# Kernel optimization log

Measured on AMD Instinct MI355X. Metric: run time of the kernel, lower is better.

Reference implementation:

```python
import jax, jax.numpy as jnp
import numpy as np

N = 100_000   # nodes
E = 3_200_000 # edges
F = 13        # input features
H = 64        # hidden dim
G = 512       # graphs in batch
C = 2         # output classes
BN_EPS = 1e-5


def _linear(key, fan_in, fan_out):
    kw, kb = jax.random.split(key)
    bound = 1.0 / np.sqrt(fan_in)
    W = jax.random.uniform(kw, (fan_in, fan_out), jnp.float32, -bound, bound)
    b = jax.random.uniform(kb, (fan_out,), jnp.float32, -bound, bound)
    return W, b


def _conv_params(key, fin, fout):
    k1, k2, k3 = jax.random.split(key, 3)
    W1, b1 = _linear(k1, fin, fout)
    W2, b2 = _linear(k2, fout, fout)
    gamma = jnp.ones((fout,), jnp.float32)
    beta = jnp.zeros((fout,), jnp.float32)
    mean = jax.random.normal(k3, (fout,), jnp.float32) * 0.1
    var = jnp.ones((fout,), jnp.float32)
    return W1, b1, gamma, beta, mean, var, W2, b2


def setup_inputs() -> dict:
    key = jax.random.key(0)
    ks = jax.random.split(key, 10)
    x = jax.random.normal(ks[0], (N, F), jnp.float32)
    src = jax.random.randint(ks[1], (E,), 0, N, jnp.int32)
    dst = jax.random.randint(ks[2], (E,), 0, N, jnp.int32)
    batch = jnp.sort(jax.random.randint(ks[3], (N,), 0, G, jnp.int32))
    inp = {"x": x, "src": src, "dst": dst, "batch": batch}
    for i, name in enumerate(["c1", "c2", "c3"]):
        fin = F if i == 0 else H
        W1, b1, g, be, m, v, W2, b2 = _conv_params(ks[4 + i], fin, H)
        inp.update({f"{name}_W1": W1, f"{name}_b1": b1, f"{name}_g": g,
                    f"{name}_be": be, f"{name}_m": m, f"{name}_v": v,
                    f"{name}_W2": W2, f"{name}_b2": b2})
    inp["fc1_W"], inp["fc1_b"] = _linear(ks[7], 3 * H, 3 * H)
    inp["fc2_W"], inp["fc2_b"] = _linear(ks[8], 3 * H, C)
    return inp


def _mlp(h, W1, b1, g, be, m, v, W2, b2):
    # Linear -> BatchNorm1d (inference, running stats) -> ReLU -> Linear -> ReLU
    h = h @ W1 + b1
    h = (h - m) * jax.lax.rsqrt(v + BN_EPS) * g + be
    h = jax.nn.relu(h)
    return jax.nn.relu(h @ W2 + b2)


def _gin_conv(x, src, dst, mlp_params):
    # GINConv with eps=0: MLP(x + sum_{j->i} x_j) via scatter-add over edges
    agg = jax.ops.segment_sum(x[src], dst, num_segments=N)
    return _mlp(x + agg, *mlp_params)


def reference(x, src, dst, batch,
              c1_W1, c1_b1, c1_g, c1_be, c1_m, c1_v, c1_W2, c1_b2,
              c2_W1, c2_b1, c2_g, c2_be, c2_m, c2_v, c2_W2, c2_b2,
              c3_W1, c3_b1, c3_g, c3_be, c3_m, c3_v, c3_W2, c3_b2,
              fc1_W, fc1_b, fc2_W, fc2_b):
    h1 = jax.nn.relu(_gin_conv(x, src, dst, (c1_W1, c1_b1, c1_g, c1_be, c1_m, c1_v, c1_W2, c1_b2)))
    h2 = jax.nn.relu(_gin_conv(h1, src, dst, (c2_W1, c2_b1, c2_g, c2_be, c2_m, c2_v, c2_W2, c2_b2)))
    h3 = jax.nn.relu(_gin_conv(h2, src, dst, (c3_W1, c3_b1, c3_g, c3_be, c3_m, c3_v, c3_W2, c3_b2)))
    p1 = jax.ops.segment_sum(h1, batch, num_segments=G)
    p2 = jax.ops.segment_sum(h2, batch, num_segments=G)
    p3 = jax.ops.segment_sum(h3, batch, num_segments=G)
    h = jnp.concatenate([p1, p2, p3], axis=1)  # [G, 3H]
    h = jax.nn.relu(h @ fc1_W + fc1_b)
    # Dropout is identity in eval mode
    h = h @ fc2_W + fc2_b
    return jax.nn.log_softmax(h, axis=-1)
```

## Files before the change

kernel.cpp:

```cpp
#include <hip/hip_runtime.h>

#define NNODES 100000
#define NEDGES 3200000
#define NF 13
#define NFP 16
#define NG 512
#define BN_EPS 1e-5f
#define NTILES (NNODES / 16)
#define CAP 72

#define BSH 9
#define NBUCK ((NNODES + 511) / 512)
#define RCAP 18500
#define PTILE 4096
#define NPBLK ((NEDGES + PTILE - 1) / PTILE)

#define NCHUNK ((NNODES + 63) / 64)
#define NPTASK (3 * NCHUNK)

typedef __attribute__((ext_vector_type(8))) _Float16 f16x8;
typedef __attribute__((ext_vector_type(4))) _Float16 f16x4;
typedef __attribute__((ext_vector_type(4))) float f32x4;

__device__ __forceinline__ unsigned short f2h(float f) {
    union { _Float16 h; unsigned short u; } c;
    c.h = (_Float16)f;
    return c.u;
}
__device__ __forceinline__ float h2f(unsigned short u) {
    union { _Float16 h; unsigned short u; } c;
    c.u = u;
    return (float)c.h;
}

__device__ __forceinline__ f16x8 shfl_xor8(f16x8 v, int m) {
    union { f16x8 h; int i[4]; } a, b;
    a.h = v;
#pragma unroll
    for (int k = 0; k < 4; ++k) b.i[k] = __shfl_xor(a.i[k], m, 64);
    return b.h;
}
__device__ __forceinline__ f16x4 shfl_xor4(f16x4 v, int m) {
    union { f16x4 h; int i[2]; } a, b;
    a.h = v;
#pragma unroll
    for (int k = 0; k < 2; ++k) b.i[k] = __shfl_xor(a.i[k], m, 64);
    return b.h;
}

__launch_bounds__(256)
__global__ void partition_kernel(const int* __restrict__ src, const int* __restrict__ dst,
                                 int* __restrict__ gcount, int* __restrict__ pairbuf) {
    __shared__ int lhist[NBUCK];
    __shared__ int lbase[NBUCK];
    __shared__ int lpos[NBUCK];
    int t = threadIdx.x;
    int base = blockIdx.x * PTILE;
    int cnt = NEDGES - base; if (cnt > PTILE) cnt = PTILE;

    int v[PTILE / 256], b[PTILE / 256];
#pragma unroll
    for (int j = 0; j < PTILE / 256; ++j) {
        int i = t + j * 256;
        if (i < cnt) {
            int d = __builtin_nontemporal_load(dst + base + i);
            int s = __builtin_nontemporal_load(src + base + i);
            b[j] = d >> BSH;
            v[j] = ((d & 511) << 17) | s;
        } else b[j] = -1;
    }
    if (t < NBUCK) lhist[t] = 0;
    __syncthreads();
#pragma unroll
    for (int j = 0; j < PTILE / 256; ++j)
        if (b[j] >= 0) atomicAdd(&lhist[b[j]], 1);
    __syncthreads();
    if (t < NBUCK) {
        lbase[t] = atomicAdd(&gcount[t], lhist[t]);
        lpos[t] = 0;
    }
    __syncthreads();
#pragma unroll
    for (int j = 0; j < PTILE / 256; ++j) {
        if (b[j] >= 0) {
            int p = atomicAdd(&lpos[b[j]], 1);
            pairbuf[(size_t)b[j] * RCAP + lbase[b[j]] + p] = v[j];
        }
    }
}

__launch_bounds__(512)
__global__ void bucket_scatter_kernel(const int* __restrict__ pairbuf,
                                      const int* __restrict__ gcount,
                                      int* __restrict__ cursor, int* __restrict__ csr) {
    __shared__ int lcnt[512];
    int bk = blockIdx.x;
    int lo = bk << BSH;
    int cnt = gcount[bk];
    if (threadIdx.x < 512) lcnt[threadIdx.x] = 0;
    __syncthreads();
    const int* pb = pairbuf + (size_t)bk * RCAP;
    for (int i = threadIdx.x; i < cnt; i += 512) {
        int p = pb[i];
        int s = p & 0x1FFFF;
        int dl = p >> 17;
        int pos = atomicAdd(&lcnt[dl], 1);
        csr[(size_t)(lo + dl) * CAP + pos] = s;
    }
    __syncthreads();
    int n = lo + threadIdx.x;
    if (threadIdx.x < 512 && n < NNODES) cursor[n] = n * CAP + lcnt[threadIdx.x];
}

__global__ void cvt_x_kernel(const float* __restrict__ x, unsigned short* __restrict__ xh) {
    const int total = NNODES * NFP;
    int idx = blockIdx.x * blockDim.x + threadIdx.x;
    int stride = gridDim.x * blockDim.x;
    for (int i = idx; i < total; i += stride) {
        int n = i >> 4;
        int f = i & 15;
        xh[i] = (f < NF) ? f2h(x[n * NF + f]) : (unsigned short)0;
    }
}

__global__ void build_frags_kernel(const float* __restrict__ w10, const float* __restrict__ w20,
                                   const float* __restrict__ w11, const float* __restrict__ w21,
                                   const float* __restrict__ w12, const float* __restrict__ w22,
                                   unsigned short* __restrict__ wfrag) {
    int tid = blockIdx.x * blockDim.x + threadIdx.x;
    if (tid >= 3072) return;
    int layer = tid >> 10;
    int rem = tid & 1023;
    int mat = rem >> 9;
    int tile = (rem >> 7) & 3;
    int chunk = (rem >> 6) & 1;
    int lane = rem & 63;
    int quad = lane >> 4, n = lane & 15;
    const float* W = (layer == 0) ? (mat ? w20 : w10)
                   : (layer == 1) ? (mat ? w21 : w11)
                                  : (mat ? w22 : w12);
    int K = (layer == 0 && mat == 0) ? NF : 64;
    unsigned short* o = wfrag + ((size_t)tid) * 8;
#pragma unroll
    for (int j = 0; j < 8; ++j) {
        int k = chunk * 32 + quad * 8 + j;
        float val = (k < K) ? W[k * 64 + tile * 16 + n] : 0.f;
        o[j] = f2h(val);
    }
}

template <int FSTR, int RL, int UNROLL, int PADZ>
__launch_bounds__(256, 8)
__global__ void agg_vec_kernel(const unsigned short* __restrict__ xin,
                               const int* __restrict__ cursor,
                               const int* __restrict__ csr,
                               unsigned short* __restrict__ y) {
    const int EPG = 64 / RL;
    int lane = threadIdx.x & 63;
    int g = lane / RL;
    int r = lane % RL;
    int wave = (blockIdx.x * blockDim.x + threadIdx.x) >> 6;
    int nw = (gridDim.x * blockDim.x) >> 6;

    for (int n = wave; n < NNODES; n += nw) {
        int beg = n * CAP;
        int end = cursor[n];
        f16x4 acc = {0, 0, 0, 0};
        if (g == 0)
            acc = *(const f16x4*)&xin[n * FSTR + r * 4];
        int j = beg;
        const int STEP = UNROLL * EPG;
        for (; j + STEP <= end; j += STEP) {
#pragma unroll
            for (int t = 0; t < UNROLL; ++t) {
                int i0 = csr[j + t * EPG + g];
                acc += *(const f16x4*)&xin[i0 * FSTR + r * 4];
            }
        }
        for (; j < end; j += EPG) {
            int e = j + g;
            if (e < end) {
                int i0 = csr[e];
                acc += *(const f16x4*)&xin[i0 * FSTR + r * 4];
            }
        }
#pragma unroll
        for (int m = RL; m < 64; m <<= 1) acc += shfl_xor4(acc, m);
        if (g == 0) {
            *(f16x4*)&y[n * 64 + r * 4] = acc;
        } else if (PADZ && g == 1) {
            f16x4 z = {0, 0, 0, 0};
            *(f16x4*)&y[n * 64 + 16 + r * 4] = z;
        }
    }
}

__launch_bounds__(256, 8)
__global__ void agg_vec8_kernel(const unsigned short* __restrict__ xin,
                                const int* __restrict__ cursor,
                                const int* __restrict__ csr,
                                unsigned short* __restrict__ y) {
    int lane = threadIdx.x & 63;
    int g = lane >> 3;
    int r = lane & 7;
    int wave = (blockIdx.x * blockDim.x + threadIdx.x) >> 6;
    int nw = (gridDim.x * blockDim.x) >> 6;

    for (int n = wave; n < NNODES; n += nw) {
        int beg = n * CAP;
        int end = cursor[n];
        f16x8 acc = {0, 0, 0, 0, 0, 0, 0, 0};
        if (g == 0)
            acc = *(const f16x8*)&xin[(size_t)n * 64 + r * 8];
        int j = beg;
        for (; j + 16 <= end; j += 16) {
#pragma unroll
            for (int t = 0; t < 2; ++t) {
                int i0 = csr[j + t * 8 + g];
                acc += *(const f16x8*)&xin[(size_t)i0 * 64 + r * 8];
            }
        }
        for (; j < end; j += 8) {
            int e = j + g;
            if (e < end) {
                int i0 = csr[e];
                acc += *(const f16x8*)&xin[(size_t)i0 * 64 + r * 8];
            }
        }
#pragma unroll
        for (int m = 8; m < 64; m <<= 1) acc += shfl_xor8(acc, m);
        if (g == 0) *(f16x8*)&y[(size_t)n * 64 + r * 8] = acc;
    }
}

template <int KC1>
__launch_bounds__(256)
__global__ void mlp_mfma_kernel(const unsigned short* __restrict__ yh,
                                const unsigned short* __restrict__ wfrag,
                                const float* __restrict__ b1, const float* __restrict__ g,
                                const float* __restrict__ be, const float* __restrict__ m,
                                const float* __restrict__ v,  const float* __restrict__ b2,
                                unsigned short* __restrict__ hout) {
    __shared__ __align__(16) unsigned short zs[4][16 * 72];
    int lane = threadIdx.x & 63;
    int wid = threadIdx.x >> 6;
    int quad = lane >> 4;
    int n16 = lane & 15;

    const f16x8* wf = (const f16x8*)wfrag;
    f16x8 w1f[4][2], w2f[4][2];
#pragma unroll
    for (int t = 0; t < 4; ++t) {
#pragma unroll
        for (int c = 0; c < 2; ++c) {
            w1f[t][c] = wf[((0 * 4 + t) * 2 + c) * 64 + lane];
            w2f[t][c] = wf[((1 * 4 + t) * 2 + c) * 64 + lane];
        }
    }
    float scaleF[4], shiftF[4], b2F[4];
#pragma unroll
    for (int t = 0; t < 4; ++t) {
        int f = t * 16 + n16;
        float sc = g[f] * rsqrtf(v[f] + BN_EPS);
        scaleF[t] = sc;
        shiftF[t] = (b1[f] - m[f]) * sc + be[f];
        b2F[t] = b2[f];
    }

    unsigned short* zrow = &zs[wid][0];
    int ntiles = gridDim.x * 4;
    for (int tile = blockIdx.x * 4 + wid; tile < NTILES; tile += ntiles) {
        int nodebase = tile * 16;
        const unsigned short* yrow = yh + (size_t)(nodebase + n16) * 64 + quad * 8;
        f16x8 a0 = *(const f16x8*)yrow;
        f16x8 a1 = (KC1 == 2) ? *(const f16x8*)(yrow + 32) : a0;

        f32x4 acc[4];
#pragma unroll
        for (int t = 0; t < 4; ++t) {
            f32x4 z4 = {0.f, 0.f, 0.f, 0.f};
            z4 = __builtin_amdgcn_mfma_f32_16x16x32_f16(a0, w1f[t][0], z4, 0, 0, 0);
            if (KC1 == 2)
                z4 = __builtin_amdgcn_mfma_f32_16x16x32_f16(a1, w1f[t][1], z4, 0, 0, 0);
            acc[t] = z4;
        }
#pragma unroll
        for (int t = 0; t < 4; ++t) {
#pragma unroll
            for (int r = 0; r < 4; ++r) {
                float z = fmaxf(fmaf(acc[t][r], scaleF[t], shiftF[t]), 0.f);
                zrow[(quad * 4 + r) * 72 + t * 16 + n16] = f2h(z);
            }
        }
        __threadfence_block();
        f16x8 az0 = *(const f16x8*)&zrow[n16 * 72 + quad * 8];
        f16x8 az1 = *(const f16x8*)&zrow[n16 * 72 + 32 + quad * 8];

        f32x4 acc2[4];
#pragma unroll
        for (int t = 0; t < 4; ++t) {
            f32x4 z4 = {0.f, 0.f, 0.f, 0.f};
            z4 = __builtin_amdgcn_mfma_f32_16x16x32_f16(az0, w2f[t][0], z4, 0, 0, 0);
            z4 = __builtin_amdgcn_mfma_f32_16x16x32_f16(az1, w2f[t][1], z4, 0, 0, 0);
            acc2[t] = z4;
        }
#pragma unroll
        for (int t = 0; t < 4; ++t) {
#pragma unroll
            for (int r = 0; r < 4; ++r) {
                float h = fmaxf(acc2[t][r] + b2F[t], 0.f);
                hout[(size_t)(nodebase + quad * 4 + r) * 64 + t * 16 + n16] = f2h(h);
            }
        }
        __threadfence_block();
    }
}

__launch_bounds__(256)
__global__ void pool_kernel(const unsigned short* __restrict__ h1,
                            const unsigned short* __restrict__ h2,
                            const unsigned short* __restrict__ h3,
                            const int* __restrict__ batch,
                            float* __restrict__ pool) {
    int task = blockIdx.x * 4 + (threadIdx.x >> 6);
    if (task >= NPTASK) return;
    int lane = threadIdx.x & 63;
    int layer = task / NCHUNK;
    int c = task - layer * NCHUNK;
    int n0 = c * 64;
    int n1 = n0 + 64; if (n1 > NNODES) n1 = NNODES;
    const unsigned short* hb = (layer == 0) ? h1 : (layer == 1) ? h2 : h3;
    float acc = 0.f;
    int curg = batch[n0];
    for (int n = n0; n < n1; ++n) {
        int gid = batch[n];
        if (gid != curg) {
            atomicAdd(&pool[(size_t)curg * 192 + layer * 64 + lane], acc);
            acc = 0.f;
            curg = gid;
        }
        acc += h2f(hb[(size_t)n * 64 + lane]);
    }
    atomicAdd(&pool[(size_t)curg * 192 + layer * 64 + lane], acc);
}

__global__ void head_kernel(const float* __restrict__ pool,
                            const float* __restrict__ fc1W, const float* __restrict__ fc1b,
                            const float* __restrict__ fc2W, const float* __restrict__ fc2b,
                            float* __restrict__ out) {
    __shared__ float ps[192];
    __shared__ float hs[192];
    int gi = blockIdx.x;
    int t = threadIdx.x;
    ps[t] = pool[gi * 192 + t];
    __syncthreads();
    float acc = fc1b[t];
#pragma unroll 8
    for (int k = 0; k < 192; ++k) acc = fmaf(ps[k], fc1W[k * 192 + t], acc);
    hs[t] = fmaxf(acc, 0.f);
    __syncthreads();
    if (t == 0) {
        float l0 = fc2b[0], l1 = fc2b[1];
        for (int k = 0; k < 192; ++k) {
            float h = hs[k];
            l0 = fmaf(h, fc2W[k * 2 + 0], l0);
            l1 = fmaf(h, fc2W[k * 2 + 1], l1);
        }
        float mx = fmaxf(l0, l1);
        float lse = mx + logf(expf(l0 - mx) + expf(l1 - mx));
        out[gi * 2 + 0] = l0 - lse;
        out[gi * 2 + 1] = l1 - lse;
    }
}

extern "C" void kernel_launch(void* const* d_in, const int* in_sizes, int n_in,
                              void* d_out, int out_size, void* d_ws, size_t ws_size,
                              hipStream_t stream) {
    const float* x = (const float*)d_in[0];
    const int* src = (const int*)d_in[1];
    const int* dst = (const int*)d_in[2];
    const int* batch = (const int*)d_in[3];
    const float* c1[8];
    const float* c2[8];
    const float* c3[8];
    for (int i = 0; i < 8; ++i) {
        c1[i] = (const float*)d_in[4 + i];
        c2[i] = (const float*)d_in[12 + i];
        c3[i] = (const float*)d_in[20 + i];
    }
    const float* fc1W = (const float*)d_in[28];
    const float* fc1b = (const float*)d_in[29];
    const float* fc2W = (const float*)d_in[30];
    const float* fc2b = (const float*)d_in[31];
    float* out = (float*)d_out;

    unsigned short* base = (unsigned short*)d_ws;
    const size_t NA = (size_t)NNODES * 64;
    unsigned short* yh  = base;
    unsigned short* xh  = yh + NA;
    unsigned short* h1  = xh + (size_t)NNODES * NFP;
    unsigned short* h2  = h1 + NA;
    unsigned short* h3  = h2 + NA;
    unsigned short* wfrag = h3 + NA;
    float* pool = (float*)(wfrag + 3 * 8192);
    int* ibase = (int*)(pool + (size_t)NG * 192);
    int* cursor  = ibase;
    int* gcount  = ibase + NNODES;
    int* csr     = gcount + NBUCK;
    int* pairbuf = csr + (size_t)NNODES * CAP + 256;

    hipMemsetAsync(gcount, 0, NBUCK * sizeof(int), stream);
    hipMemsetAsync(pool, 0, (size_t)NG * 192 * sizeof(float), stream);

    cvt_x_kernel<<<2048, 256, 0, stream>>>(x, xh);
    build_frags_kernel<<<12, 256, 0, stream>>>(c1[0], c1[6], c2[0], c2[6], c3[0], c3[6], wfrag);
    partition_kernel<<<NPBLK, 256, 0, stream>>>(src, dst, gcount, pairbuf);
    bucket_scatter_kernel<<<NBUCK, 512, 0, stream>>>(pairbuf, gcount, cursor, csr);

    const int AGG_BLOCKS = 25000;
    const int MLP_BLOCKS = 1024;

    agg_vec_kernel<NFP, 4, 2, 1><<<AGG_BLOCKS, 256, 0, stream>>>(xh, cursor, csr, yh);
    mlp_mfma_kernel<1><<<MLP_BLOCKS, 256, 0, stream>>>(
        yh, wfrag + 0 * 8192, c1[1], c1[2], c1[3], c1[4], c1[5], c1[7], h1);

    agg_vec8_kernel<<<AGG_BLOCKS, 256, 0, stream>>>(h1, cursor, csr, yh);
    mlp_mfma_kernel<2><<<MLP_BLOCKS, 256, 0, stream>>>(
        yh, wfrag + 1 * 8192, c2[1], c2[2], c2[3], c2[4], c2[5], c2[7], h2);

    agg_vec8_kernel<<<AGG_BLOCKS, 256, 0, stream>>>(h2, cursor, csr, yh);
    mlp_mfma_kernel<2><<<MLP_BLOCKS, 256, 0, stream>>>(
        yh, wfrag + 2 * 8192, c3[1], c3[2], c3[3], c3[4], c3[5], c3[7], h3);

    pool_kernel<<<(NPTASK + 3) / 4, 256, 0, stream>>>(h1, h2, h3, batch, pool);
    head_kernel<<<NG, 192, 0, stream>>>(pool, fc1W, fc1b, fc2W, fc2b, out);
}
```

Baseline: 407.3 us.

## Pad CSR rows with zero-node sentinel and batch two nodes per wave in aggregation

Each node's CSR row is now padded to a multiple of 8 and at least 48 entries with a sentinel index that points at an extra all-zero feature row appended to each feature buffer. The aggregation kernels can then issue all index loads and gathers for the first 48 neighbours unconditionally. Each wave also processes two nodes at once, so more independent memory requests are in flight. The cost is extra sentinel gathers and padding writes, higher register pressure (launch bounds lowered to 4), and half as many blocks.

Measured after the change: 467.8 us. 1.15x slower.

```diff
diff --git a/kernel.cpp b/kernel.cpp
--- a/kernel.cpp
+++ b/kernel.cpp
@@ -8,6 +8,7 @@
 #define BN_EPS 1e-5f
 #define NTILES (NNODES / 16)
 #define CAP 72
+#define ZERON NNODES
 
 #define BSH 9
 #define NBUCK ((NNODES + 511) / 512)
@@ -109,7 +110,13 @@
     }
     __syncthreads();
     int n = lo + threadIdx.x;
-    if (threadIdx.x < 512 && n < NNODES) cursor[n] = n * CAP + lcnt[threadIdx.x];
+    if (threadIdx.x < 512 && n < NNODES) {
+        int deg = lcnt[threadIdx.x];
+        int padded = (deg + 7) & ~7;
+        if (padded < 48) padded = 48;
+        for (int p = deg; p < padded; ++p) csr[(size_t)n * CAP + p] = ZERON;
+        cursor[n] = n * CAP + padded;
+    }
 }
 
 __global__ void cvt_x_kernel(const float* __restrict__ x, unsigned short* __restrict__ xh) {
@@ -126,8 +133,17 @@
 __global__ void build_frags_kernel(const float* __restrict__ w10, const float* __restrict__ w20,
                                    const float* __restrict__ w11, const float* __restrict__ w21,
                                    const float* __restrict__ w12, const float* __restrict__ w22,
-                                   unsigned short* __restrict__ wfrag) {
+                                   unsigned short* __restrict__ wfrag,
+                                   unsigned short* __restrict__ xh,
+                                   unsigned short* __restrict__ h1,
+                                   unsigned short* __restrict__ h2) {
     int tid = blockIdx.x * blockDim.x + threadIdx.x;
+    if (blockIdx.x == 0 && threadIdx.x < 64) {
+        int t = threadIdx.x;
+        if (t < 16) xh[(size_t)NNODES * NFP + t] = 0;
+        h1[(size_t)NNODES * 64 + t] = 0;
+        h2[(size_t)NNODES * 64 + t] = 0;
+    }
     if (tid >= 3072) return;
     int layer = tid >> 10;
     int rem = tid & 1023;
@@ -149,53 +165,71 @@
     }
 }
 
-template <int FSTR, int RL, int UNROLL, int PADZ>
-__launch_bounds__(256, 8)
+template <int FSTR, int PADZ>
+__launch_bounds__(256, 4)
 __global__ void agg_vec_kernel(const unsigned short* __restrict__ xin,
                                const int* __restrict__ cursor,
                                const int* __restrict__ csr,
                                unsigned short* __restrict__ y) {
-    const int EPG = 64 / RL;
     int lane = threadIdx.x & 63;
-    int g = lane / RL;
-    int r = lane % RL;
+    int g = lane >> 2;
+    int r = lane & 3;
     int wave = (blockIdx.x * blockDim.x + threadIdx.x) >> 6;
     int nw = (gridDim.x * blockDim.x) >> 6;
 
-    for (int n = wave; n < NNODES; n += nw) {
-        int beg = n * CAP;
-        int end = cursor[n];
-        f16x4 acc = {0, 0, 0, 0};
-        if (g == 0)
-            acc = *(const f16x4*)&xin[n * FSTR + r * 4];
-        int j = beg;
-        const int STEP = UNROLL * EPG;
-        for (; j + STEP <= end; j += STEP) {
-#pragma unroll
-            for (int t = 0; t < UNROLL; ++t) {
-                int i0 = csr[j + t * EPG + g];
-                acc += *(const f16x4*)&xin[i0 * FSTR + r * 4];
-            }
-        }
-        for (; j < end; j += EPG) {
+    for (int n0 = wave * 2; n0 < NNODES; n0 += nw * 2) {
+        int nA = n0, nB = n0 + 1;
+        int baseA = nA * CAP, baseB = nB * CAP;
+        int endA = cursor[nA], endB = cursor[nB];
+
+        int idxA[3], idxB[3];
+#pragma unroll
+        for (int t = 0; t < 3; ++t) idxA[t] = csr[baseA + t * 16 + g];
+#pragma unroll
+        for (int t = 0; t < 3; ++t) idxB[t] = csr[baseB + t * 16 + g];
+        f16x4 vA[3], vB[3];
+#pragma unroll
+        for (int t = 0; t < 3; ++t) vA[t] = *(const f16x4*)&xin[(size_t)idxA[t] * FSTR + r * 4];
+#pragma unroll
+        for (int t = 0; t < 3; ++t) vB[t] = *(const f16x4*)&xin[(size_t)idxB[t] * FSTR + r * 4];
+
+        f16x4 accA = {0, 0, 0, 0};
+        f16x4 accB = {0, 0, 0, 0};
+        if (g == 0) {
+            accA = *(const f16x4*)&xin[(size_t)nA * FSTR + r * 4];
+            accB = *(const f16x4*)&xin[(size_t)nB * FSTR + r * 4];
+        }
+#pragma unroll
+        for (int t = 0; t < 3; ++t) { accA += vA[t]; accB += vB[t]; }
+
+        for (int j = baseA + 48; j < endA; j += 16) {
             int e = j + g;
-            if (e < end) {
-                int i0 = csr[e];
-                acc += *(const f16x4*)&xin[i0 * FSTR + r * 4];
-            }
-        }
-#pragma unroll
-        for (int m = RL; m < 64; m <<= 1) acc += shfl_xor4(acc, m);
+            int i0 = (e < endA) ? csr[e] : ZERON;
+            accA += *(const f16x4*)&xin[(size_t)i0 * FSTR + r * 4];
+        }
+        for (int j = baseB + 48; j < endB; j += 16) {
+            int e = j + g;
+            int i0 = (e < endB) ? csr[e] : ZERON;
+            accB += *(const f16x4*)&xin[(size_t)i0 * FSTR + r * 4];
+        }
+
+#pragma unroll
+        for (int m = 4; m < 64; m <<= 1) {
+            accA += shfl_xor4(accA, m);
+            accB += shfl_xor4(accB, m);
+        }
         if (g == 0) {
-            *(f16x4*)&y[n * 64 + r * 4] = acc;
+            *(f16x4*)&y[(size_t)nA * 64 + r * 4] = accA;
+            *(f16x4*)&y[(size_t)nB * 64 + r * 4] = accB;
         } else if (PADZ && g == 1) {
             f16x4 z = {0, 0, 0, 0};
-            *(f16x4*)&y[n * 64 + 16 + r * 4] = z;
-        }
-    }
-}
-
-__launch_bounds__(256, 8)
+            *(f16x4*)&y[(size_t)nA * 64 + 16 + r * 4] = z;
+            *(f16x4*)&y[(size_t)nB * 64 + 16 + r * 4] = z;
+        }
+    }
+}
+
+__launch_bounds__(256, 4)
 __global__ void agg_vec8_kernel(const unsigned short* __restrict__ xin,
                                 const int* __restrict__ cursor,
                                 const int* __restrict__ csr,
@@ -206,30 +240,49 @@
     int wave = (blockIdx.x * blockDim.x + threadIdx.x) >> 6;
     int nw = (gridDim.x * blockDim.x) >> 6;
 
-    for (int n = wave; n < NNODES; n += nw) {
-        int beg = n * CAP;
-        int end = cursor[n];
-        f16x8 acc = {0, 0, 0, 0, 0, 0, 0, 0};
-        if (g == 0)
-            acc = *(const f16x8*)&xin[(size_t)n * 64 + r * 8];
-        int j = beg;
-        for (; j + 16 <= end; j += 16) {
-#pragma unroll
-            for (int t = 0; t < 2; ++t) {
-                int i0 = csr[j + t * 8 + g];
-                acc += *(const f16x8*)&xin[(size_t)i0 * 64 + r * 8];
-            }
-        }
-        for (; j < end; j += 8) {
-            int e = j + g;
-            if (e < end) {
-                int i0 = csr[e];
-                acc += *(const f16x8*)&xin[(size_t)i0 * 64 + r * 8];
-            }
-        }
-#pragma unroll
-        for (int m = 8; m < 64; m <<= 1) acc += shfl_xor8(acc, m);
-        if (g == 0) *(f16x8*)&y[(size_t)n * 64 + r * 8] = acc;
+    for (int n0 = wave * 2; n0 < NNODES; n0 += nw * 2) {
+        int nA = n0, nB = n0 + 1;
+        int baseA = nA * CAP, baseB = nB * CAP;
+        int endA = cursor[nA], endB = cursor[nB];
+
+        int idxA[6], idxB[6];
+#pragma unroll
+        for (int t = 0; t < 6; ++t) idxA[t] = csr[baseA + t * 8 + g];
+#pragma unroll
+        for (int t = 0; t < 6; ++t) idxB[t] = csr[baseB + t * 8 + g];
+        f16x8 vA[6], vB[6];
+#pragma unroll
+        for (int t = 0; t < 6; ++t) vA[t] = *(const f16x8*)&xin[(size_t)idxA[t] * 64 + r * 8];
+#pragma unroll
+        for (int t = 0; t < 6; ++t) vB[t] = *(const f16x8*)&xin[(size_t)idxB[t] * 64 + r * 8];
+
+        f16x8 accA = {0, 0, 0, 0, 0, 0, 0, 0};
+        f16x8 accB = {0, 0, 0, 0, 0, 0, 0, 0};
+        if (g == 0) {
+            accA = *(const f16x8*)&xin[(size_t)nA * 64 + r * 8];
+            accB = *(const f16x8*)&xin[(size_t)nB * 64 + r * 8];
+        }
+#pragma unroll
+        for (int t = 0; t < 6; ++t) { accA += vA[t]; accB += vB[t]; }
+
+        for (int j = baseA + 48; j < endA; j += 8) {
+            int i0 = csr[j + g];
+            accA += *(const f16x8*)&xin[(size_t)i0 * 64 + r * 8];
+        }
+        for (int j = baseB + 48; j < endB; j += 8) {
+            int i0 = csr[j + g];
+            accB += *(const f16x8*)&xin[(size_t)i0 * 64 + r * 8];
+        }
+
+#pragma unroll
+        for (int m = 8; m < 64; m <<= 1) {
+            accA += shfl_xor8(accA, m);
+            accB += shfl_xor8(accB, m);
+        }
+        if (g == 0) {
+            *(f16x8*)&y[(size_t)nA * 64 + r * 8] = accA;
+            *(f16x8*)&y[(size_t)nB * 64 + r * 8] = accB;
+        }
     }
 }
 
@@ -396,11 +449,12 @@
 
     unsigned short* base = (unsigned short*)d_ws;
     const size_t NA = (size_t)NNODES * 64;
+    const size_t NA1 = (size_t)(NNODES + 1) * 64;
     unsigned short* yh  = base;
     unsigned short* xh  = yh + NA;
-    unsigned short* h1  = xh + (size_t)NNODES * NFP;
-    unsigned short* h2  = h1 + NA;
-    unsigned short* h3  = h2 + NA;
+    unsigned short* h1  = xh + (size_t)(NNODES + 1) * NFP;
+    unsigned short* h2  = h1 + NA1;
+    unsigned short* h3  = h2 + NA1;
     unsigned short* wfrag = h3 + NA;
     float* pool = (float*)(wfrag + 3 * 8192);
     int* ibase = (int*)(pool + (size_t)NG * 192);
@@ -413,14 +467,15 @@
     hipMemsetAsync(pool, 0, (size_t)NG * 192 * sizeof(float), stream);
 
     cvt_x_kernel<<<2048, 256, 0, stream>>>(x, xh);
-    build_frags_kernel<<<12, 256, 0, stream>>>(c1[0], c1[6], c2[0], c2[6], c3[0], c3[6], wfrag);
+    build_frags_kernel<<<12, 256, 0, stream>>>(c1[0], c1[6], c2[0], c2[6], c3[0], c3[6],
+                                               wfrag, xh, h1, h2);
     partition_kernel<<<NPBLK, 256, 0, stream>>>(src, dst, gcount, pairbuf);
     bucket_scatter_kernel<<<NBUCK, 512, 0, stream>>>(pairbuf, gcount, cursor, csr);
 
-    const int AGG_BLOCKS = 25000;
+    const int AGG_BLOCKS = 12500;
     const int MLP_BLOCKS = 1024;
 
-    agg_vec_kernel<NFP, 4, 2, 1><<<AGG_BLOCKS, 256, 0, stream>>>(xh, cursor, csr, yh);
+    agg_vec_kernel<NFP, 1><<<AGG_BLOCKS, 256, 0, stream>>>(xh, cursor, csr, yh);
     mlp_mfma_kernel<1><<<MLP_BLOCKS, 256, 0, stream>>>(
         yh, wfrag + 0 * 8192, c1[1], c1[2], c1[3], c1[4], c1[5], c1[7], h1);
 
```
